# Optimization experiments

Measured on AMD Instinct MI355X. Metric: run time of the kernel, lower is better.

Reference implementation:

```python
import jax, jax.numpy as jnp
import numpy as np

# Soft boolean gate arithmetic (exact on {0,1} inputs, matches typical SNN gate semantics):
#   OR(a,b)  = a + b - a*b  (chained ORs == 1 - prod(1-x))
#   AND(a,b) = a*b
#   NOT(a)   = 1 - a
#   XOR(a,b) = a + b - 2*a*b
#   MUX(sel, a, b) = sel*a + (1-sel)*b   (sel==1 picks a)

def _or(a, b):
    return a + b - a * b

def _and(a, b):
    return a * b

def _not(a):
    return 1.0 - a

def _xor(a, b):
    return a + b - 2.0 * a * b

def _mux(sel, a, b):
    return sel * a + (1.0 - sel) * b


def setup_inputs() -> dict:
    key = jax.random.key(0)
    N = 4194304
    bits = jax.random.randint(key, (N, 16), 0, 2).astype(jnp.float32)
    return {"fp16_pulse": bits}


def reference(fp16_pulse):
    x = fp16_pulse
    batch = x.shape[:-1]
    s = x[..., 0:1]
    e4, e3, e2, e1, e0 = (x[..., i:i + 1] for i in range(1, 6))
    m = x[..., 6:16]  # [M9..M0]
    zeros = jnp.zeros_like(s)
    ones = jnp.ones_like(s)

    # exponent zero / all-ones detection
    e_nonzero = _or(_or(_or(e0, e1), _or(e2, e3)), e4)
    e_is_zero = _not(e_nonzero)
    e_is_max = _and(_and(_and(e0, e1), _and(e2, e3)), e4)

    # mantissa nonzero: tree of ORs == 1 - prod(1 - m_i)
    m_nonzero = 1.0 - jnp.prod(1.0 - m, axis=-1, keepdims=True)
    not_m_nz = _not(m_nonzero)

    is_zero = _and(e_is_zero, not_m_nz)
    is_subnormal = _and(e_is_zero, m_nonzero)
    is_inf = _and(e_is_max, not_m_nz)
    is_nan = _and(e_is_max, m_nonzero)

    # 8-bit ripple-carry adder, LSB-first: exp16 + 112 (bias diff 127-15)
    a_bits = [e0, e1, e2, e3, e4, zeros, zeros, zeros]
    b_bits = [zeros, zeros, zeros, zeros, ones, ones, ones, zeros]  # 112 = 0b01110000
    carry = zeros
    sum_bits = []
    for i in range(8):
        p = _xor(a_bits[i], b_bits[i])
        sum_bits.append(_xor(p, carry))
        carry = _or(_and(a_bits[i], b_bits[i]), _and(p, carry))
    fp32_exp_normal = jnp.concatenate(sum_bits[::-1], axis=-1)  # MSB-first [E7..E0]

    zeros13 = jnp.zeros(batch + (13,), dtype=x.dtype)
    zeros23 = jnp.zeros(batch + (23,), dtype=x.dtype)
    ones8 = jnp.ones(batch + (8,), dtype=x.dtype)
    fp32_mant_normal = jnp.concatenate([m, zeros13], axis=-1)  # [M22..M0]

    # subnormal -> zeros (simplified, as in source)
    exp_sel = (1.0 - is_subnormal) * fp32_exp_normal
    mant_sel = (1.0 - is_subnormal) * fp32_mant_normal
    em_sel = jnp.concatenate([exp_sel, mant_sel], axis=-1)  # [...,31]

    after_zero = (1.0 - is_zero) * em_sel

    inf_result = jnp.concatenate([ones8, zeros23], axis=-1)
    after_inf = _mux(is_inf, inf_result, after_zero)

    nan_result = jnp.concatenate([ones8, m, zeros13], axis=-1)
    after_nan = _mux(is_nan, nan_result, after_inf)

    return jnp.concatenate([s, after_nan], axis=-1)  # [...,32]
```

## Files before the change

### kernel.cpp

```cpp
#include <hip/hip_runtime.h>

__global__ __launch_bounds__(256) void fp16_to_fp32_bits_kernel(
    const float* __restrict__ in, float* __restrict__ out, int n) {
    int tid = blockIdx.x * blockDim.x + threadIdx.x;
    int stride = gridDim.x * blockDim.x;
    for (int i = tid; i < n; i += stride) {
        const float4* ip = reinterpret_cast<const float4*>(in + (size_t)i * 16);
        float4 v0 = ip[0];
        float4 v1 = ip[1];
        float4 v2 = ip[2];
        float4 v3 = ip[3];
        float b[16] = {v0.x, v0.y, v0.z, v0.w, v1.x, v1.y, v1.z, v1.w,
                       v2.x, v2.y, v2.z, v2.w, v3.x, v3.y, v3.z, v3.w};

        unsigned E = 0u;
#pragma unroll
        for (int k = 0; k < 5; ++k) E = (E << 1) | (b[1 + k] != 0.0f ? 1u : 0u);

        unsigned exp8 = (E == 31u) ? 255u : ((E == 0u) ? 0u : E + 112u);
        float msc = (E == 0u) ? 0.0f : 1.0f;

        float o[32];
        o[0] = b[0];
#pragma unroll
        for (int k = 0; k < 8; ++k) o[1 + k] = (float)((exp8 >> (7 - k)) & 1u);
#pragma unroll
        for (int j = 0; j < 10; ++j) o[9 + j] = b[6 + j] * msc;
#pragma unroll
        for (int j = 19; j < 32; ++j) o[j] = 0.0f;

        float4* op = reinterpret_cast<float4*>(out + (size_t)i * 32);
#pragma unroll
        for (int k = 0; k < 8; ++k)
            op[k] = make_float4(o[4 * k], o[4 * k + 1], o[4 * k + 2], o[4 * k + 3]);
    }
}

extern "C" void kernel_launch(void* const* d_in, const int* in_sizes, int n_in,
                              void* d_out, int out_size, void* d_ws, size_t ws_size,
                              hipStream_t stream) {
    const float* in = (const float*)d_in[0];
    float* out = (float*)d_out;
    int n = in_sizes[0] / 16;
    int block = 256;
    int maxBlocks = 2048;
    int blocks = (n + block - 1) / block;
    if (blocks > maxBlocks) blocks = maxBlocks;
    fp16_to_fp32_bits_kernel<<<blocks, block, 0, stream>>>(in, out, n);
}
```

Measured before the change: 803.9 us.

## Split each row across eight lanes with shuffle-assembled bitmask for coalesced I/O

Work is remapped so that 8 consecutive lanes share one 16-bit input row. Each lane loads 8 bytes and writes one float4 of the 32-float output. The lanes OR their bits together with xor-shuffles into a packed bitmask, and bit reversal builds the exponent and output bits with integer ops. The goal is fully coalesced loads and stores in place of the per-thread 64B/128B strided accesses. In exchange it adds shuffle traffic and assumes that lane groups of 8 stay active together in the grid-stride loop.

```diff
diff --git a/kernel.cpp b/kernel.cpp
--- a/kernel.cpp
+++ b/kernel.cpp
@@ -1,50 +1,40 @@
 #include <hip/hip_runtime.h>
 
 __global__ __launch_bounds__(256) void fp16_to_fp32_bits_kernel(
-    const float* __restrict__ in, float* __restrict__ out, int n) {
+    const uint2* __restrict__ in, float4* __restrict__ out, int n_tasks) {
     int tid = blockIdx.x * blockDim.x + threadIdx.x;
     int stride = gridDim.x * blockDim.x;
-    for (int i = tid; i < n; i += stride) {
-        const float4* ip = reinterpret_cast<const float4*>(in + (size_t)i * 16);
-        float4 v0 = ip[0];
-        float4 v1 = ip[1];
-        float4 v2 = ip[2];
-        float4 v3 = ip[3];
-        float b[16] = {v0.x, v0.y, v0.z, v0.w, v1.x, v1.y, v1.z, v1.w,
-                       v2.x, v2.y, v2.z, v2.w, v3.x, v3.y, v3.z, v3.w};
+    for (int g = tid; g < n_tasks; g += stride) {
+        uint2 u = in[g];
+        unsigned q = (unsigned)g & 7u;
+        unsigned local = ((u.x ? 1u : 0u) | (u.y ? 2u : 0u)) << (2u * q);
+        local |= __shfl_xor((int)local, 1);
+        local |= __shfl_xor((int)local, 2);
+        local |= __shfl_xor((int)local, 4);
 
-        unsigned E = 0u;
-#pragma unroll
-        for (int k = 0; k < 5; ++k) E = (E << 1) | (b[1 + k] != 0.0f ? 1u : 0u);
+        unsigned E = __brev(local >> 1) >> 27;
+        unsigned exp8 = (E == 31u) ? 255u : ((E == 0u) ? 0u : E + 112u);
+        unsigned mmask = (E == 0u) ? 0u : 0x3FFu;
 
-        unsigned exp8 = (E == 31u) ? 255u : ((E == 0u) ? 0u : E + 112u);
-        float msc = (E == 0u) ? 0.0f : 1.0f;
+        unsigned obits = (local & 1u)
+                       | ((__brev(exp8) >> 24) << 1)
+                       | (((local >> 6) & mmask) << 9);
 
-        float o[32];
-        o[0] = b[0];
-#pragma unroll
-        for (int k = 0; k < 8; ++k) o[1 + k] = (float)((exp8 >> (7 - k)) & 1u);
-#pragma unroll
-        for (int j = 0; j < 10; ++j) o[9 + j] = b[6 + j] * msc;
-#pragma unroll
-        for (int j = 19; j < 32; ++j) o[j] = 0.0f;
-
-        float4* op = reinterpret_cast<float4*>(out + (size_t)i * 32);
-#pragma unroll
-        for (int k = 0; k < 8; ++k)
-            op[k] = make_float4(o[4 * k], o[4 * k + 1], o[4 * k + 2], o[4 * k + 3]);
+        unsigned nib = (obits >> (4u * q)) & 0xFu;
+        out[g] = make_float4((float)(nib & 1u), (float)((nib >> 1) & 1u),
+                             (float)((nib >> 2) & 1u), (float)((nib >> 3) & 1u));
     }
 }
 
 extern "C" void kernel_launch(void* const* d_in, const int* in_sizes, int n_in,
                               void* d_out, int out_size, void* d_ws, size_t ws_size,
                               hipStream_t stream) {
-    const float* in = (const float*)d_in[0];
-    float* out = (float*)d_out;
-    int n = in_sizes[0] / 16;
+    const uint2* in = (const uint2*)d_in[0];
+    float4* out = (float4*)d_out;
+    int n_tasks = in_sizes[0] / 2;
     int block = 256;
     int maxBlocks = 2048;
-    int blocks = (n + block - 1) / block;
+    int blocks = (n_tasks + block - 1) / block;
     if (blocks > maxBlocks) blocks = maxBlocks;
-    fp16_to_fp32_bits_kernel<<<blocks, block, 0, stream>>>(in, out, n);
+    fp16_to_fp32_bits_kernel<<<blocks, block, 0, stream>>>(in, out, n_tasks);
 }
```

New measurement: 676.5 us, median of 2. -15.8%, faster.
